# Kernel optimization log

Hardware: AMD Instinct MI355X
Metric: run time of the kernel (lower is better)

## Reference

```python
import jax, jax.numpy as jnp
import numpy as np

N_NODES = 100000
N_EDGES = 3200000
BATCH = 16
LAYER_NUMBER = 4


def setup_inputs() -> dict:
    key = jax.random.key(0)
    k1, k2, k3, k4 = jax.random.split(key, 4)
    x = jax.random.normal(k1, (N_NODES, BATCH), dtype=jnp.float32)
    # learnable per-edge weights (log1p(counts) at init in the original; the
    # parameter itself is what is learned, so a plain random init is faithful)
    weights = jax.random.normal(k2, (N_EDGES,), dtype=jnp.float32)
    row = jax.random.randint(k3, (N_EDGES,), 0, N_NODES, dtype=jnp.int64)
    col = jax.random.randint(k4, (N_EDGES,), 0, N_NODES, dtype=jnp.int64)
    return {"x": x, "weights": weights, "row": row, "col": col}


def reference(x, weights, row, col):
    # Repeated sparse COO SpMM: y <- A @ y, applied layer_number times,
    # where A[row[e], col[e]] = weights[e].
    def step(y, _):
        msg = weights[:, None] * y[col]                      # [E, B] gather + scale
        y_new = jax.ops.segment_sum(msg, row, num_segments=N_NODES)  # [N, B] scatter-add
        return y_new, None

    y, _ = jax.lax.scan(step, x, None, length=LAYER_NUMBER)
    return y
```

## Files before the change

kernel.cpp:

```cpp
#include <hip/hip_runtime.h>

#define N_NODES 100000
#define N_EDGES 3200000
#define BATCH 16
#define BKT_SHIFT 6
#define BKT_NODES 64
#define K_BUCKETS 1563
#define NB 256
#define SUB (N_EDGES / NB)
#define FT 512
#define SCAN_T 256
#define SCAN_C 7
#define CAP 4096
#define PD 12

__global__ void hist_kernel(const int* __restrict__ row, int* __restrict__ blk_cnt) {
    __shared__ int lh[K_BUCKETS];
    int t = threadIdx.x, blk = blockIdx.x;
    for (int k = t; k < K_BUCKETS; k += 256) lh[k] = 0;
    __syncthreads();
    int base = blk * SUB;
    for (int e = base + t; e < base + SUB; e += 256)
        atomicAdd(&lh[row[e] >> BKT_SHIFT], 1);
    __syncthreads();
    for (int k = t; k < K_BUCKETS; k += 256)
        blk_cnt[k * NB + blk] = lh[k];
}

__global__ void colscan_kernel(int* __restrict__ blk_cnt, int* __restrict__ totals) {
    int bkt = blockIdx.x * blockDim.x + threadIdx.x;
    if (bkt >= K_BUCKETS) return;
    int4* p = (int4*)&blk_cnt[bkt * NB];
    int acc = 0;
    for (int q = 0; q < NB / 4; q++) {
        int4 v = p[q];
        int4 o;
        o.x = acc; acc += v.x;
        o.y = acc; acc += v.y;
        o.z = acc; acc += v.z;
        o.w = acc; acc += v.w;
        p[q] = o;
    }
    totals[bkt] = acc;
}

__global__ void scan_kernel(const int* __restrict__ totals, int* __restrict__ bptr,
                            int* __restrict__ row_ptr) {
    __shared__ int s[SCAN_T];
    int t = threadIdx.x;
    int loc[SCAN_C];
    int sum = 0;
    for (int i = 0; i < SCAN_C; i++) {
        int idx = t * SCAN_C + i;
        int v = (idx < K_BUCKETS) ? totals[idx] : 0;
        loc[i] = v;
        sum += v;
    }
    s[t] = sum;
    __syncthreads();
    for (int off = 1; off < SCAN_T; off <<= 1) {
        int x = (t >= off) ? s[t - off] : 0;
        __syncthreads();
        s[t] += x;
        __syncthreads();
    }
    int excl = s[t] - sum;
    for (int i = 0; i < SCAN_C; i++) {
        int idx = t * SCAN_C + i;
        if (idx < K_BUCKETS) bptr[idx] = excl;
        excl += loc[i];
    }
    if (t == 0) { bptr[K_BUCKETS] = N_EDGES; row_ptr[N_NODES] = N_EDGES; }
}

__global__ void __launch_bounds__(FT) fill_kernel(
        const int* __restrict__ row, const int* __restrict__ col,
        const float* __restrict__ w,
        const int* __restrict__ bptr, const int* __restrict__ blk_cnt,
        uint2* __restrict__ entries) {
    __shared__ uint2 sbuf[SUB];
    __shared__ int lbeg[K_BUCKETS];
    __shared__ int lcur[K_BUCKETS];
    __shared__ int sscan[FT];
    int t = threadIdx.x, blk = blockIdx.x;
    for (int k = t; k < K_BUCKETS; k += FT) lcur[k] = 0;
    __syncthreads();
    int base = blk * SUB;
    for (int e = base + t; e < base + SUB; e += FT)
        atomicAdd(&lcur[row[e] >> BKT_SHIFT], 1);
    __syncthreads();
    int loc[4];
    int sum = 0;
    #pragma unroll
    for (int j = 0; j < 4; j++) {
        int k = t * 4 + j;
        int v = (k < K_BUCKETS) ? lcur[k] : 0;
        loc[j] = v;
        sum += v;
    }
    sscan[t] = sum;
    __syncthreads();
    for (int off = 1; off < FT; off <<= 1) {
        int x = (t >= off) ? sscan[t - off] : 0;
        __syncthreads();
        sscan[t] += x;
        __syncthreads();
    }
    int excl = sscan[t] - sum;
    #pragma unroll
    for (int j = 0; j < 4; j++) {
        int k = t * 4 + j;
        if (k < K_BUCKETS) { lbeg[k] = excl; lcur[k] = excl; }
        excl += loc[j];
    }
    __syncthreads();
    for (int e = base + t; e < base + SUB; e += FT) {
        int r = row[e];
        int bkt = r >> BKT_SHIFT;
        int pos = atomicAdd(&lcur[bkt], 1);
        sbuf[pos] = make_uint2(((unsigned)(r & (BKT_NODES - 1)) << 17) | (unsigned)col[e],
                               __float_as_uint(w[e]));
    }
    __syncthreads();
    int lane = t & 7;
    for (int k = (t >> 3); k < K_BUCKETS; k += FT / 8) {
        int lb = lbeg[k];
        int le = lcur[k];
        int dst = bptr[k] + blk_cnt[k * NB + blk];
        for (int i = lb + lane; i < le; i += 8)
            entries[dst + (i - lb)] = sbuf[i];
    }
}

__global__ void nodesort_kernel(const int* __restrict__ bptr, uint2* __restrict__ entries,
                                int* __restrict__ row_ptr) {
    __shared__ uint2 ebuf[CAP];
    __shared__ int nh[BKT_NODES];
    __shared__ int nc[BKT_NODES];
    int t = threadIdx.x, b = blockIdx.x;
    int beg = bptr[b], end = bptr[b + 1];
    int n = min(end - beg, CAP);
    if (t < BKT_NODES) nh[t] = 0;
    __syncthreads();
    for (int k = t; k < n; k += 256) {
        uint2 r = entries[beg + k];
        ebuf[k] = r;
        atomicAdd(&nh[r.x >> 17], 1);
    }
    __syncthreads();
    if (t == 0) {
        int acc = 0;
        for (int i = 0; i < BKT_NODES; i++) {
            int v = nh[i];
            int node = b * BKT_NODES + i;
            if (node < N_NODES) row_ptr[node] = beg + acc;
            nc[i] = acc;
            acc += v;
        }
    }
    __syncthreads();
    for (int k = t; k < n; k += 256) {
        uint2 r = ebuf[k];
        int pos = atomicAdd(&nc[r.x >> 17], 1);
        entries[beg + pos] = r;
    }
}

__global__ void __launch_bounds__(256) pull_kernel(const float* __restrict__ y,
                            const uint2* __restrict__ entries,
                            const int* __restrict__ row_ptr,
                            float* __restrict__ out) {
    int tid = blockIdx.x * blockDim.x + threadIdx.x;
    int node = tid >> 4;
    int b = tid & 15;
    if (node >= N_NODES) return;
    int beg = row_ptr[node];
    int end = row_ptr[node + 1];
    float acc = 0.f;
    if (beg < end) {
        int lim = end - 1;
        uint2 r[PD];
        #pragma unroll
        for (int j = 0; j < PD; j++) r[j] = entries[min(beg + j, lim)];
        int i = beg;
        while (i + PD <= end) {
            float yv[PD];
            #pragma unroll
            for (int j = 0; j < PD; j++)
                yv[j] = y[(r[j].x & 0x1FFFFu) * BATCH + b];
            uint2 nx[PD];
            #pragma unroll
            for (int j = 0; j < PD; j++)
                nx[j] = entries[min(i + PD + j, lim)];
            #pragma unroll
            for (int j = 0; j < PD; j++)
                acc += __uint_as_float(r[j].y) * yv[j];
            #pragma unroll
            for (int j = 0; j < PD; j++) r[j] = nx[j];
            i += PD;
        }
        if (i < end) {
            float yv[PD];
            #pragma unroll
            for (int j = 0; j < PD; j++)
                yv[j] = y[(r[j].x & 0x1FFFFu) * BATCH + b];
            #pragma unroll
            for (int j = 0; j < PD; j++)
                if (i + j < end)
                    acc += __uint_as_float(r[j].y) * yv[j];
        }
    }
    out[node * BATCH + b] = acc;
}

extern "C" void kernel_launch(void* const* d_in, const int* in_sizes, int n_in,
                              void* d_out, int out_size, void* d_ws, size_t ws_size,
                              hipStream_t stream) {
    const float* x   = (const float*)d_in[0];
    const float* w   = (const float*)d_in[1];
    const int*   row = (const int*)d_in[2];
    const int*   col = (const int*)d_in[3];
    float*       out = (float*)d_out;

    char* p = (char*)d_ws;
    uint2* entries = (uint2*)p;  p += (size_t)N_EDGES * sizeof(uint2);
    float* buf     = (float*)p;
    int*   blk_cnt = (int*)buf;
    p += (size_t)N_NODES * BATCH * sizeof(float);
    int* totals  = (int*)p;      p += 8192;
    int* bptr    = (int*)p;      p += 8192;
    int* row_ptr = (int*)p;

    hist_kernel<<<NB, 256, 0, stream>>>(row, blk_cnt);
    colscan_kernel<<<(K_BUCKETS + 255) / 256, 256, 0, stream>>>(blk_cnt, totals);
    scan_kernel<<<1, SCAN_T, 0, stream>>>(totals, bptr, row_ptr);
    fill_kernel<<<NB, FT, 0, stream>>>(row, col, w, bptr, blk_cnt, entries);
    nodesort_kernel<<<K_BUCKETS, 256, 0, stream>>>(bptr, entries, row_ptr);

    const int pgrid = (N_NODES * BATCH + 255) / 256;
    pull_kernel<<<pgrid, 256, 0, stream>>>(x,   entries, row_ptr, buf);
    pull_kernel<<<pgrid, 256, 0, stream>>>(buf, entries, row_ptr, out);
    pull_kernel<<<pgrid, 256, 0, stream>>>(out, entries, row_ptr, buf);
    pull_kernel<<<pgrid, 256, 0, stream>>>(buf, entries, row_ptr, out);
}
```

Before: 368.4 us.

## Parallelize histogram and column-scan preprocessing, widen nodesort blocks, shrink pull prefetch

The histogram kernel now runs four blocks per edge slice and merges their counts into a zeroed global table with atomics. The column scan is now spread over 16 threads per bucket with a shared-memory segment scan, where before one thread scanned each bucket alone. Nodesort uses 512 threads per block, and the pull kernel's prefetch depth goes from 12 to 8. The goal is more parallelism in the small preprocessing kernels. The cost is an extra memset, global atomics, and possibly less memory-level parallelism in the pull loop.

```diff
diff --git a/kernel.cpp b/kernel.cpp
--- a/kernel.cpp
+++ b/kernel.cpp
@@ -8,40 +8,76 @@
 #define K_BUCKETS 1563
 #define NB 256
 #define SUB (N_EDGES / NB)
+#define HSPLIT 4
+#define HSUB (SUB / HSPLIT)
 #define FT 512
 #define SCAN_T 256
 #define SCAN_C 7
 #define CAP 4096
-#define PD 12
+#define NT 512
+#define PD 8
+#define CS_BPB 16
 
 __global__ void hist_kernel(const int* __restrict__ row, int* __restrict__ blk_cnt) {
     __shared__ int lh[K_BUCKETS];
     int t = threadIdx.x, blk = blockIdx.x;
+    int s = blk >> 2;
+    int q = blk & 3;
     for (int k = t; k < K_BUCKETS; k += 256) lh[k] = 0;
     __syncthreads();
-    int base = blk * SUB;
-    for (int e = base + t; e < base + SUB; e += 256)
+    int base = s * SUB + q * HSUB;
+    for (int e = base + t; e < base + HSUB; e += 256)
         atomicAdd(&lh[row[e] >> BKT_SHIFT], 1);
     __syncthreads();
-    for (int k = t; k < K_BUCKETS; k += 256)
-        blk_cnt[k * NB + blk] = lh[k];
+    for (int k = t; k < K_BUCKETS; k += 256) {
+        int v = lh[k];
+        if (v) atomicAdd(&blk_cnt[k * NB + s], v);
+    }
 }
 
 __global__ void colscan_kernel(int* __restrict__ blk_cnt, int* __restrict__ totals) {
-    int bkt = blockIdx.x * blockDim.x + threadIdx.x;
-    if (bkt >= K_BUCKETS) return;
-    int4* p = (int4*)&blk_cnt[bkt * NB];
-    int acc = 0;
-    for (int q = 0; q < NB / 4; q++) {
-        int4 v = p[q];
-        int4 o;
-        o.x = acc; acc += v.x;
-        o.y = acc; acc += v.y;
-        o.z = acc; acc += v.z;
-        o.w = acc; acc += v.w;
-        p[q] = o;
-    }
-    totals[bkt] = acc;
+    __shared__ int seg[CS_BPB][16];
+    int t = threadIdx.x;
+    int lb = t >> 4;
+    int sg = t & 15;
+    int bkt = blockIdx.x * CS_BPB + lb;
+    bool ok = bkt < K_BUCKETS;
+    int4 v[4];
+    int sum = 0;
+    int4* p = nullptr;
+    if (ok) {
+        p = (int4*)&blk_cnt[bkt * NB + sg * 16];
+        #pragma unroll
+        for (int qq = 0; qq < 4; qq++) {
+            v[qq] = p[qq];
+            sum += v[qq].x + v[qq].y + v[qq].z + v[qq].w;
+        }
+    }
+    seg[lb][sg] = sum;
+    __syncthreads();
+    if (sg == 0 && ok) {
+        int acc = 0;
+        #pragma unroll
+        for (int i = 0; i < 16; i++) {
+            int x = seg[lb][i];
+            seg[lb][i] = acc;
+            acc += x;
+        }
+        totals[bkt] = acc;
+    }
+    __syncthreads();
+    if (ok) {
+        int acc = seg[lb][sg];
+        #pragma unroll
+        for (int qq = 0; qq < 4; qq++) {
+            int4 o;
+            o.x = acc; acc += v[qq].x;
+            o.y = acc; acc += v[qq].y;
+            o.z = acc; acc += v[qq].z;
+            o.w = acc; acc += v[qq].w;
+            p[qq] = o;
+        }
+    }
 }
 
 __global__ void scan_kernel(const int* __restrict__ totals, int* __restrict__ bptr,
@@ -132,8 +168,9 @@
     }
 }
 
-__global__ void nodesort_kernel(const int* __restrict__ bptr, uint2* __restrict__ entries,
-                                int* __restrict__ row_ptr) {
+__global__ void __launch_bounds__(NT) nodesort_kernel(
+        const int* __restrict__ bptr, uint2* __restrict__ entries,
+        int* __restrict__ row_ptr) {
     __shared__ uint2 ebuf[CAP];
     __shared__ int nh[BKT_NODES];
     __shared__ int nc[BKT_NODES];
@@ -142,7 +179,7 @@
     int n = min(end - beg, CAP);
     if (t < BKT_NODES) nh[t] = 0;
     __syncthreads();
-    for (int k = t; k < n; k += 256) {
+    for (int k = t; k < n; k += NT) {
         uint2 r = entries[beg + k];
         ebuf[k] = r;
         atomicAdd(&nh[r.x >> 17], 1);
@@ -159,7 +196,7 @@
         }
     }
     __syncthreads();
-    for (int k = t; k < n; k += 256) {
+    for (int k = t; k < n; k += NT) {
         uint2 r = ebuf[k];
         int pos = atomicAdd(&nc[r.x >> 17], 1);
         entries[beg + pos] = r;
@@ -231,11 +268,12 @@
     int* bptr    = (int*)p;      p += 8192;
     int* row_ptr = (int*)p;
 
-    hist_kernel<<<NB, 256, 0, stream>>>(row, blk_cnt);
-    colscan_kernel<<<(K_BUCKETS + 255) / 256, 256, 0, stream>>>(blk_cnt, totals);
+    hipMemsetAsync(blk_cnt, 0, (size_t)K_BUCKETS * NB * sizeof(int), stream);
+    hist_kernel<<<NB * HSPLIT, 256, 0, stream>>>(row, blk_cnt);
+    colscan_kernel<<<(K_BUCKETS + CS_BPB - 1) / CS_BPB, 256, 0, stream>>>(blk_cnt, totals);
     scan_kernel<<<1, SCAN_T, 0, stream>>>(totals, bptr, row_ptr);
     fill_kernel<<<NB, FT, 0, stream>>>(row, col, w, bptr, blk_cnt, entries);
-    nodesort_kernel<<<K_BUCKETS, 256, 0, stream>>>(bptr, entries, row_ptr);
+    nodesort_kernel<<<K_BUCKETS, NT, 0, stream>>>(bptr, entries, row_ptr);
 
     const int pgrid = (N_NODES * BATCH + 255) / 256;
     pull_kernel<<<pgrid, 256, 0, stream>>>(x,   entries, row_ptr, buf);
```

New measurement: 387.5 us. +5.2%, slower.
